# Optimization experiments

Hardware: AMD Instinct MI355X
Metric: run time of the kernel (lower is better)

## Reference

```python
import jax, jax.numpy as jnp
import numpy as np

N, E, D, K = 50000, 600000, 128, 8
EPS = 1e-09


def setup_inputs() -> dict:
    key = jax.random.key(0)
    ks = jax.random.split(key, 10)
    feature = jax.random.normal(ks[0], (N, D), dtype=jnp.float32)
    snorm_n = jax.random.uniform(ks[1], (N, 1), dtype=jnp.float32)
    src = jax.random.randint(ks[2], (E,), 0, N, dtype=jnp.int32)
    dst = jax.random.randint(ks[3], (E,), 0, N, dtype=jnp.int32)
    W_low = jax.random.normal(ks[4], (D, D), dtype=jnp.float32) / np.sqrt(D)
    W_high = jax.random.normal(ks[5], (D, D), dtype=jnp.float32) / np.sqrt(D)
    W_mid = jax.random.normal(ks[6], (D, D), dtype=jnp.float32) / np.sqrt(D)
    gamma_low = jax.random.uniform(ks[7], (K,), dtype=jnp.float32)
    gamma_high = jax.random.uniform(ks[8], (K,), dtype=jnp.float32)
    gamma_mid = jax.random.uniform(ks[9], (K,), dtype=jnp.float32)
    bias = jnp.zeros((D,), dtype=jnp.float32)
    return {"feature": feature, "snorm_n": snorm_n, "src": src, "dst": dst,
            "W_low": W_low, "W_high": W_high, "W_mid": W_mid,
            "gamma_low": gamma_low, "gamma_high": gamma_high,
            "gamma_mid": gamma_mid, "bias": bias}


def _mp(feat, src, dst, norm):
    # symmetric-normalized SpMM: h[v] = norm[v] * sum_{u->v} norm[u]*feat[u]
    msg = (feat * norm[:, None])[src]                        # [E, D] gather
    agg = jax.ops.segment_sum(msg, dst, num_segments=N)       # [N, D] scatter-add
    return agg * norm[:, None]


def reference(feature, snorm_n, src, dst, W_low, W_high, W_mid,
              gamma_low, gamma_high, gamma_mid, bias):
    deg = jax.ops.segment_sum(jnp.ones((E,), feature.dtype), dst, num_segments=N)
    norm = jnp.clip(deg, 1.0) ** -0.5                          # in-degree^-0.5
    alpha = jnp.linspace(EPS, 1.0 - EPS, K).astype(feature.dtype)
    midalpha = jnp.linspace(EPS, 1.0, K).astype(feature.dtype)

    h = _mp(feature, src, dst, norm)

    gl = jax.nn.relu(gamma_low)
    o0 = (jnp.dot(alpha, gl) * h + jnp.dot(1.0 - alpha, gl) * feature) @ W_low.T
    gh = jax.nn.relu(gamma_high)
    o1 = (jnp.dot(-alpha, gh) * h + jnp.dot(1.0 - alpha, gh) * feature) @ W_high.T
    gm = jax.nn.relu(gamma_mid)
    h1 = _mp(h, src, dst, norm)
    o2 = (jnp.sum(gm) * h1 - jnp.dot(midalpha, gm) * feature) @ W_mid.T

    # sequential mutual gating, exactly as the torch in-place updates
    o0 = o0 * jax.nn.sigmoid(o1 + o2)
    o1 = o1 * jax.nn.sigmoid(o0 + o2)
    o2 = o2 * jax.nn.sigmoid(o0 + o1)

    out = o0 + o1 + o2 + bias
    out = out * snorm_n          # graph_norm
    out = jax.nn.relu(out)       # activation
    return out
```

## Files before the change

kernel.cpp:

```cpp
#include <hip/hip_runtime.h>
#include <hip/hip_bf16.h>
#include <math.h>

#define N_NODES 50000
#define N_EDGES 600000
#define DIM 128
#define KGAM 8
#define EPSV 1e-9f

typedef __attribute__((ext_vector_type(8))) short short8;
typedef __attribute__((ext_vector_type(4))) float float4v;

__device__ __forceinline__ float bf2f(short s) {
    unsigned int u = ((unsigned int)(unsigned short)s) << 16;
    return __builtin_bit_cast(float, u);
}
__device__ __forceinline__ short f2bf(float f) {
    return (short)__builtin_bit_cast(unsigned short, __float2bfloat16(f));
}
__device__ __forceinline__ unsigned int pack2(float a, float b) {
    return (unsigned int)(unsigned short)f2bf(a) | ((unsigned int)(unsigned short)f2bf(b) << 16);
}
__device__ __forceinline__ float sigm(float x) { return 1.f / (1.f + __expf(-x)); }

__global__ void k_zero_int(int* __restrict__ p, int n) {
    int i = blockIdx.x * blockDim.x + threadIdx.x;
    if (i < n) p[i] = 0;
}

__global__ void k_deg(const int* __restrict__ dst, int* __restrict__ deg) {
    int e = blockIdx.x * blockDim.x + threadIdx.x;
    if (e < N_EDGES) atomicAdd(&deg[dst[e]], 1);
}

__global__ void k_scan1(const int* __restrict__ deg, int* __restrict__ rowstart,
                        int* __restrict__ bsums, float* __restrict__ norm) {
    __shared__ int s[256];
    int tid = threadIdx.x;
    int i0 = blockIdx.x * 1024 + tid * 4;
    int v[4]; int sum = 0;
#pragma unroll
    for (int c = 0; c < 4; ++c) {
        int i = i0 + c;
        int d = (i < N_NODES) ? deg[i] : 0;
        v[c] = d; sum += d;
    }
    s[tid] = sum; __syncthreads();
#pragma unroll
    for (int off = 1; off < 256; off <<= 1) {
        int t = (tid >= off) ? s[tid - off] : 0;
        __syncthreads();
        s[tid] += t;
        __syncthreads();
    }
    if (tid == 255) bsums[blockIdx.x] = s[255];
    int run = s[tid] - sum;
#pragma unroll
    for (int c = 0; c < 4; ++c) {
        int i = i0 + c;
        if (i < N_NODES) {
            rowstart[i] = run;
            norm[i] = rsqrtf((float)(v[c] < 1 ? 1 : v[c]));
        }
        run += v[c];
    }
}

__global__ void k_scan2(int* __restrict__ bsums, int nb) {
    __shared__ int s[64];
    int tid = threadIdx.x;
    int v = (tid < nb) ? bsums[tid] : 0;
    s[tid] = v; __syncthreads();
#pragma unroll
    for (int off = 1; off < 64; off <<= 1) {
        int t = (tid >= off) ? s[tid - off] : 0;
        __syncthreads();
        s[tid] += t;
        __syncthreads();
    }
    if (tid < nb) bsums[tid] = s[tid] - v;
}

__global__ void k_scan3(const int* __restrict__ bsums, int* __restrict__ rowstart) {
    int i = blockIdx.x * blockDim.x + threadIdx.x;
    if (i < N_NODES) rowstart[i] += bsums[i >> 10];
    if (i == 0) rowstart[N_NODES] = N_EDGES;
}

__global__ void k_fill(const int* __restrict__ src, const int* __restrict__ dst,
                       const int* __restrict__ rowstart, int* __restrict__ cnt,
                       int* __restrict__ esrc) {
    int e = blockIdx.x * blockDim.x + threadIdx.x;
    if (e < N_EDGES) {
        int d = dst[e];
        int slot = rowstart[d] + atomicAdd(&cnt[d], 1);
        esrc[slot] = src[e];
    }
}

__global__ void k_coeffs(const float* __restrict__ gl, const float* __restrict__ gh,
                         const float* __restrict__ gm, float* __restrict__ c) {
    if (threadIdx.x == 0 && blockIdx.x == 0) {
        float a0 = 0, b0 = 0, a1 = 0, b1 = 0, sg = 0, m2 = 0;
        for (int k = 0; k < KGAM; ++k) {
            float al = EPSV + (float)k * (1.f - 2.f * EPSV) / (KGAM - 1);
            float md = EPSV + (float)k * (1.f - EPSV) / (KGAM - 1);
            float l = fmaxf(gl[k], 0.f), h = fmaxf(gh[k], 0.f), m = fmaxf(gm[k], 0.f);
            a0 += al * l;  b0 += (1.f - al) * l;
            a1 += -al * h; b1 += (1.f - al) * h;
            sg += m;       m2 += md * m;
        }
        c[0] = a0; c[1] = b0; c[2] = a1; c[3] = b1; c[4] = sg; c[5] = -m2;
    }
}

__global__ void k_wconv(const float* __restrict__ W0, const float* __restrict__ W1,
                        const float* __restrict__ W2, const float* __restrict__ coeffs,
                        unsigned int* __restrict__ Wb) {
    int g = blockIdx.y;
    const float* Ws = (g < 2) ? W0 : (g < 4) ? W1 : W2;
    float c = coeffs[g];
    int i = (blockIdx.x * 256 + threadIdx.x) * 4;
    if (i < DIM * DIM) {
        float4 v = *(const float4*)(Ws + i);
        uint2 o; o.x = pack2(c * v.x, c * v.y); o.y = pack2(c * v.z, c * v.w);
        *(uint2*)(Wb + (g * DIM * DIM + i) / 2) = o;
    }
}

__global__ void k_prescale(const float4* __restrict__ f, const float* __restrict__ norm,
                           uint2* __restrict__ fb, uint2* __restrict__ fp) {
    int i = blockIdx.x * 256 + threadIdx.x;
    if (i >= N_NODES * DIM / 4) return;
    int row = i >> 5;
    float nv = norm[row];
    float4 v = f[i];
    uint2 a; a.x = pack2(v.x, v.y); a.y = pack2(v.z, v.w);
    uint2 b; b.x = pack2(v.x * nv, v.y * nv); b.y = pack2(v.z * nv, v.w * nv);
    fb[i] = a;
    fp[i] = b;
}

__device__ __forceinline__ void acc8(float* a, uint4 r) {
    a[0] += __builtin_bit_cast(float, r.x << 16);
    a[1] += __builtin_bit_cast(float, r.x & 0xffff0000u);
    a[2] += __builtin_bit_cast(float, r.y << 16);
    a[3] += __builtin_bit_cast(float, r.y & 0xffff0000u);
    a[4] += __builtin_bit_cast(float, r.z << 16);
    a[5] += __builtin_bit_cast(float, r.z & 0xffff0000u);
    a[6] += __builtin_bit_cast(float, r.w << 16);
    a[7] += __builtin_bit_cast(float, r.w & 0xffff0000u);
}

__global__ void k_spmm(const uint4* __restrict__ in, const float* __restrict__ norm,
                       const int* __restrict__ rowstart, const int* __restrict__ esrc,
                       uint4* __restrict__ hout, uint4* __restrict__ preout, int wpre) {
    int v = blockIdx.x * 16 + (threadIdx.x >> 4);
    int l = threadIdx.x & 15;
    if (v >= N_NODES) return;
    int beg = rowstart[v], end = rowstart[v + 1];
    float a[8] = {0.f, 0.f, 0.f, 0.f, 0.f, 0.f, 0.f, 0.f};
    int t = beg;
    for (; t + 3 < end; t += 4) {
        int u0 = esrc[t], u1 = esrc[t + 1], u2 = esrc[t + 2], u3 = esrc[t + 3];
        uint4 r0 = in[(size_t)u0 * 16 + l];
        uint4 r1 = in[(size_t)u1 * 16 + l];
        uint4 r2 = in[(size_t)u2 * 16 + l];
        uint4 r3 = in[(size_t)u3 * 16 + l];
        acc8(a, r0); acc8(a, r1); acc8(a, r2); acc8(a, r3);
    }
    for (; t < end; ++t) {
        uint4 r = in[(size_t)esrc[t] * 16 + l];
        acc8(a, r);
    }
    float nv = norm[v];
    uint4 o;
    o.x = pack2(a[0] * nv, a[1] * nv); o.y = pack2(a[2] * nv, a[3] * nv);
    o.z = pack2(a[4] * nv, a[5] * nv); o.w = pack2(a[6] * nv, a[7] * nv);
    hout[(size_t)v * 16 + l] = o;
    if (wpre) {
        float n2 = nv * nv;
        uint4 p;
        p.x = pack2(a[0] * n2, a[1] * n2); p.y = pack2(a[2] * n2, a[3] * n2);
        p.z = pack2(a[4] * n2, a[5] * n2); p.w = pack2(a[6] * n2, a[7] * n2);
        preout[(size_t)v * 16 + l] = p;
    }
}

#define RT 64

__global__ __launch_bounds__(512, 4) void k_gemm_fused(
    const short* __restrict__ hB, const short* __restrict__ fB,
    const short* __restrict__ h1B, const short* __restrict__ Wb,
    const float* __restrict__ bias, const float* __restrict__ snorm,
    float* __restrict__ out) {
    const int r0 = blockIdx.x * RT;
    const int tid = threadIdx.x;
    const int lane = tid & 63;
    const int ct = tid >> 6;
    const int m = lane & 15;
    const int quad = lane >> 4;

    float4v acc[3][4];
    const float4v zero = {0.f, 0.f, 0.f, 0.f};
#pragma unroll
    for (int g = 0; g < 3; ++g)
#pragma unroll
        for (int rt = 0; rt < 4; ++rt) acc[g][rt] = zero;

    const short* ah = hB  + (size_t)(r0 + m) * DIM + quad * 8;
    const short* af = fB  + (size_t)(r0 + m) * DIM + quad * 8;
    const short* a1 = h1B + (size_t)(r0 + m) * DIM + quad * 8;
    const short* wp = Wb  + (size_t)(ct * 16 + m) * DIM + quad * 8;

#pragma unroll
    for (int ks = 0; ks < 4; ++ks) {
        const int ko = ks * 32;
        short8 b0 = *(const short8*)(wp + ko);
        short8 b1 = *(const short8*)(wp + ko + DIM * DIM);
        short8 b2 = *(const short8*)(wp + ko + 2 * DIM * DIM);
        short8 b3 = *(const short8*)(wp + ko + 3 * DIM * DIM);
        short8 b4 = *(const short8*)(wp + ko + 4 * DIM * DIM);
        short8 b5 = *(const short8*)(wp + ko + 5 * DIM * DIM);
#pragma unroll
        for (int rt = 0; rt < 4; ++rt) {
            const int ro = rt * 16 * DIM + ko;
            short8 x_h = *(const short8*)(ah + ro);
            short8 x_f = *(const short8*)(af + ro);
            short8 x_1 = *(const short8*)(a1 + ro);
            acc[0][rt] = __builtin_amdgcn_mfma_f32_16x16x32_bf16(x_h, b0, acc[0][rt], 0, 0, 0);
            acc[0][rt] = __builtin_amdgcn_mfma_f32_16x16x32_bf16(x_f, b1, acc[0][rt], 0, 0, 0);
            acc[1][rt] = __builtin_amdgcn_mfma_f32_16x16x32_bf16(x_h, b2, acc[1][rt], 0, 0, 0);
            acc[1][rt] = __builtin_amdgcn_mfma_f32_16x16x32_bf16(x_f, b3, acc[1][rt], 0, 0, 0);
            acc[2][rt] = __builtin_amdgcn_mfma_f32_16x16x32_bf16(x_1, b4, acc[2][rt], 0, 0, 0);
            acc[2][rt] = __builtin_amdgcn_mfma_f32_16x16x32_bf16(x_f, b5, acc[2][rt], 0, 0, 0);
        }
    }

    const int col = ct * 16 + m;
    const float bc = bias[col];
#pragma unroll
    for (int rt = 0; rt < 4; ++rt) {
#pragma unroll
        for (int r = 0; r < 4; ++r) {
            int row = r0 + rt * 16 + quad * 4 + r;
            if (row < N_NODES) {
                float sn = snorm[row];
                float o0 = acc[0][rt][r], o1 = acc[1][rt][r], o2 = acc[2][rt][r];
                float g0 = o0 * sigm(o1 + o2);
                float g1 = o1 * sigm(g0 + o2);
                float g2 = o2 * sigm(g0 + g1);
                float vv = (g0 + g1 + g2 + bc) * sn;
                out[(size_t)row * DIM + col] = fmaxf(vv, 0.f);
            }
        }
    }
}

extern "C" void kernel_launch(void* const* d_in, const int* in_sizes, int n_in,
                              void* d_out, int out_size, void* d_ws, size_t ws_size,
                              hipStream_t stream) {
    const float* feature = (const float*)d_in[0];
    const float* snorm   = (const float*)d_in[1];
    const int*   src     = (const int*)d_in[2];
    const int*   dst     = (const int*)d_in[3];
    const float* W_low   = (const float*)d_in[4];
    const float* W_high  = (const float*)d_in[5];
    const float* W_mid   = (const float*)d_in[6];
    const float* gl      = (const float*)d_in[7];
    const float* gh      = (const float*)d_in[8];
    const float* gm      = (const float*)d_in[9];
    const float* bias    = (const float*)d_in[10];
    float* out = (float*)d_out;

    char* w = (char*)d_ws;
    auto alloc = [&](size_t bytes) {
        char* p = w;
        w += (bytes + 255) & ~(size_t)255;
        return p;
    };
    float* norm   = (float*)alloc((size_t)N_NODES * 4);
    int* deg      = (int*)alloc((size_t)2 * N_NODES * 4);
    int* cnt      = deg + N_NODES;
    int* rowstart = (int*)alloc((size_t)(N_NODES + 1) * 4);
    int* bsums    = (int*)alloc(64 * 4);
    int* esrc     = (int*)alloc((size_t)N_EDGES * 4);
    float* coeffs = (float*)alloc(64 * 4);
    short* Wb     = (short*)alloc((size_t)6 * DIM * DIM * 2);
    short* fb     = (short*)alloc((size_t)N_NODES * DIM * 2);
    short* fp     = (short*)alloc((size_t)N_NODES * DIM * 2);
    short* h      = (short*)alloc((size_t)N_NODES * DIM * 2);
    short* hp     = (short*)alloc((size_t)N_NODES * DIM * 2);
    short* h1     = (short*)alloc((size_t)N_NODES * DIM * 2);

    k_zero_int<<<(2 * N_NODES + 255) / 256, 256, 0, stream>>>(deg, 2 * N_NODES);
    k_deg<<<(N_EDGES + 255) / 256, 256, 0, stream>>>(dst, deg);
    int nchunks = (N_NODES + 1023) / 1024;
    k_scan1<<<nchunks, 256, 0, stream>>>(deg, rowstart, bsums, norm);
    k_scan2<<<1, 64, 0, stream>>>(bsums, nchunks);
    k_scan3<<<(N_NODES + 255) / 256, 256, 0, stream>>>(bsums, rowstart);
    k_fill<<<(N_EDGES + 255) / 256, 256, 0, stream>>>(src, dst, rowstart, cnt, esrc);
    k_coeffs<<<1, 1, 0, stream>>>(gl, gh, gm, coeffs);
    k_wconv<<<dim3(16, 6), 256, 0, stream>>>(W_low, W_high, W_mid, coeffs,
                                             (unsigned int*)Wb);
    k_prescale<<<(N_NODES * DIM / 4 + 255) / 256, 256, 0, stream>>>(
        (const float4*)feature, norm, (uint2*)fb, (uint2*)fp);

    int spmm_blocks = (N_NODES + 15) / 16;
    k_spmm<<<spmm_blocks, 256, 0, stream>>>((const uint4*)fp, norm, rowstart, esrc,
                                            (uint4*)h, (uint4*)hp, 1);
    k_spmm<<<spmm_blocks, 256, 0, stream>>>((const uint4*)hp, norm, rowstart, esrc,
                                            (uint4*)h1, (uint4*)hp, 0);

    k_gemm_fused<<<(N_NODES + RT - 1) / RT, 512, 0, stream>>>(
        h, fb, h1, Wb, bias, snorm, out);
}
```

Before: 288.7 us.

## Stage GEMM activations in LDS, unroll SpMM by 8, fold coeffs into wconv

The fused GEMM kernel now loads the block's h, feature and h1 tiles into shared memory once via global_load_lds. Previously all 8 waves re-read the same activation rows from global memory. The SpMM gather loop is unrolled to 8 outstanding row loads, with a 4/2/1 tail, to expose more memory parallelism. The single-thread coefficient kernel is folded into k_wconv and the zeroing kernel is replaced by hipMemsetAsync, removing two launches. The GEMM now uses 48KB of LDS per block, which may limit occupancy.

```diff
diff --git a/kernel.cpp b/kernel.cpp
--- a/kernel.cpp
+++ b/kernel.cpp
@@ -11,10 +11,6 @@
 typedef __attribute__((ext_vector_type(8))) short short8;
 typedef __attribute__((ext_vector_type(4))) float float4v;
 
-__device__ __forceinline__ float bf2f(short s) {
-    unsigned int u = ((unsigned int)(unsigned short)s) << 16;
-    return __builtin_bit_cast(float, u);
-}
 __device__ __forceinline__ short f2bf(float f) {
     return (short)__builtin_bit_cast(unsigned short, __float2bfloat16(f));
 }
@@ -22,11 +18,6 @@
     return (unsigned int)(unsigned short)f2bf(a) | ((unsigned int)(unsigned short)f2bf(b) << 16);
 }
 __device__ __forceinline__ float sigm(float x) { return 1.f / (1.f + __expf(-x)); }
-
-__global__ void k_zero_int(int* __restrict__ p, int n) {
-    int i = blockIdx.x * blockDim.x + threadIdx.x;
-    if (i < n) p[i] = 0;
-}
 
 __global__ void k_deg(const int* __restrict__ dst, int* __restrict__ deg) {
     int e = blockIdx.x * blockDim.x + threadIdx.x;
@@ -98,28 +89,24 @@
     }
 }
 
-__global__ void k_coeffs(const float* __restrict__ gl, const float* __restrict__ gh,
-                         const float* __restrict__ gm, float* __restrict__ c) {
-    if (threadIdx.x == 0 && blockIdx.x == 0) {
-        float a0 = 0, b0 = 0, a1 = 0, b1 = 0, sg = 0, m2 = 0;
-        for (int k = 0; k < KGAM; ++k) {
-            float al = EPSV + (float)k * (1.f - 2.f * EPSV) / (KGAM - 1);
-            float md = EPSV + (float)k * (1.f - EPSV) / (KGAM - 1);
-            float l = fmaxf(gl[k], 0.f), h = fmaxf(gh[k], 0.f), m = fmaxf(gm[k], 0.f);
-            a0 += al * l;  b0 += (1.f - al) * l;
-            a1 += -al * h; b1 += (1.f - al) * h;
-            sg += m;       m2 += md * m;
-        }
-        c[0] = a0; c[1] = b0; c[2] = a1; c[3] = b1; c[4] = sg; c[5] = -m2;
-    }
-}
-
 __global__ void k_wconv(const float* __restrict__ W0, const float* __restrict__ W1,
-                        const float* __restrict__ W2, const float* __restrict__ coeffs,
+                        const float* __restrict__ W2, const float* __restrict__ gl,
+                        const float* __restrict__ gh, const float* __restrict__ gm,
                         unsigned int* __restrict__ Wb) {
     int g = blockIdx.y;
+    float a0 = 0, b0 = 0, a1 = 0, b1 = 0, sg = 0, m2 = 0;
+#pragma unroll
+    for (int k = 0; k < KGAM; ++k) {
+        float al = EPSV + (float)k * (1.f - 2.f * EPSV) / (KGAM - 1);
+        float md = EPSV + (float)k * (1.f - EPSV) / (KGAM - 1);
+        float l = fmaxf(gl[k], 0.f), h = fmaxf(gh[k], 0.f), m = fmaxf(gm[k], 0.f);
+        a0 += al * l;  b0 += (1.f - al) * l;
+        a1 += -al * h; b1 += (1.f - al) * h;
+        sg += m;       m2 += md * m;
+    }
+    float cc[6] = {a0, b0, a1, b1, sg, -m2};
+    float c = cc[g];
     const float* Ws = (g < 2) ? W0 : (g < 4) ? W1 : W2;
-    float c = coeffs[g];
     int i = (blockIdx.x * 256 + threadIdx.x) * 4;
     if (i < DIM * DIM) {
         float4 v = *(const float4*)(Ws + i);
@@ -161,15 +148,37 @@
     int beg = rowstart[v], end = rowstart[v + 1];
     float a[8] = {0.f, 0.f, 0.f, 0.f, 0.f, 0.f, 0.f, 0.f};
     int t = beg;
-    for (; t + 3 < end; t += 4) {
+    for (; t + 7 < end; t += 8) {
+        int u0 = esrc[t],     u1 = esrc[t + 1], u2 = esrc[t + 2], u3 = esrc[t + 3];
+        int u4 = esrc[t + 4], u5 = esrc[t + 5], u6 = esrc[t + 6], u7 = esrc[t + 7];
+        uint4 r0 = in[(size_t)u0 * 16 + l];
+        uint4 r1 = in[(size_t)u1 * 16 + l];
+        uint4 r2 = in[(size_t)u2 * 16 + l];
+        uint4 r3 = in[(size_t)u3 * 16 + l];
+        uint4 r4 = in[(size_t)u4 * 16 + l];
+        uint4 r5 = in[(size_t)u5 * 16 + l];
+        uint4 r6 = in[(size_t)u6 * 16 + l];
+        uint4 r7 = in[(size_t)u7 * 16 + l];
+        acc8(a, r0); acc8(a, r1); acc8(a, r2); acc8(a, r3);
+        acc8(a, r4); acc8(a, r5); acc8(a, r6); acc8(a, r7);
+    }
+    if (t + 3 < end) {
         int u0 = esrc[t], u1 = esrc[t + 1], u2 = esrc[t + 2], u3 = esrc[t + 3];
         uint4 r0 = in[(size_t)u0 * 16 + l];
         uint4 r1 = in[(size_t)u1 * 16 + l];
         uint4 r2 = in[(size_t)u2 * 16 + l];
         uint4 r3 = in[(size_t)u3 * 16 + l];
         acc8(a, r0); acc8(a, r1); acc8(a, r2); acc8(a, r3);
-    }
-    for (; t < end; ++t) {
+        t += 4;
+    }
+    if (t + 1 < end) {
+        int u0 = esrc[t], u1 = esrc[t + 1];
+        uint4 r0 = in[(size_t)u0 * 16 + l];
+        uint4 r1 = in[(size_t)u1 * 16 + l];
+        acc8(a, r0); acc8(a, r1);
+        t += 2;
+    }
+    if (t < end) {
         uint4 r = in[(size_t)esrc[t] * 16 + l];
         acc8(a, r);
     }
@@ -189,18 +198,36 @@
 
 #define RT 64
 
+typedef const __attribute__((address_space(1))) unsigned int* gp1_t;
+typedef __attribute__((address_space(3))) unsigned int* lp3_t;
+
 __global__ __launch_bounds__(512, 4) void k_gemm_fused(
     const short* __restrict__ hB, const short* __restrict__ fB,
     const short* __restrict__ h1B, const short* __restrict__ Wb,
     const float* __restrict__ bias, const float* __restrict__ snorm,
     float* __restrict__ out) {
+    __shared__ short Ts[48 * 512];
+
     const int r0 = blockIdx.x * RT;
     const int tid = threadIdx.x;
     const int lane = tid & 63;
-    const int ct = tid >> 6;
+    const int wv = tid >> 6;
     const int m = lane & 15;
     const int quad = lane >> 4;
 
+#pragma unroll
+    for (int i = 0; i < 6; ++i) {
+        int s = wv * 6 + i;
+        int g = s >> 4, rt = (s >> 2) & 3, ks = s & 3;
+        const short* base = (g == 0) ? hB : (g == 1) ? fB : h1B;
+        int row = r0 + rt * 16 + m;
+        row = (row < N_NODES) ? row : (N_NODES - 1);
+        const short* gp = base + (size_t)row * DIM + ks * 32 + quad * 8;
+        __builtin_amdgcn_global_load_lds((gp1_t)(const void*)gp,
+                                         (lp3_t)(void*)&Ts[s * 512], 16, 0, 0);
+    }
+    __syncthreads();
+
     float4v acc[3][4];
     const float4v zero = {0.f, 0.f, 0.f, 0.f};
 #pragma unroll
@@ -208,11 +235,7 @@
 #pragma unroll
         for (int rt = 0; rt < 4; ++rt) acc[g][rt] = zero;
 
-    const short* ah = hB  + (size_t)(r0 + m) * DIM + quad * 8;
-    const short* af = fB  + (size_t)(r0 + m) * DIM + quad * 8;
-    const short* a1 = h1B + (size_t)(r0 + m) * DIM + quad * 8;
-    const short* wp = Wb  + (size_t)(ct * 16 + m) * DIM + quad * 8;
-
+    const short* wp = Wb + (size_t)(wv * 16 + m) * DIM + quad * 8;
 #pragma unroll
     for (int ks = 0; ks < 4; ++ks) {
         const int ko = ks * 32;
@@ -224,10 +247,10 @@
         short8 b5 = *(const short8*)(wp + ko + 5 * DIM * DIM);
 #pragma unroll
         for (int rt = 0; rt < 4; ++rt) {
-            const int ro = rt * 16 * DIM + ko;
-            short8 x_h = *(const short8*)(ah + ro);
-            short8 x_f = *(const short8*)(af + ro);
-            short8 x_1 = *(const short8*)(a1 + ro);
+            const short* ap = &Ts[(rt * 4 + ks) * 512 + lane * 8];
+            short8 x_h = *(const short8*)(ap);
+            short8 x_f = *(const short8*)(ap + 16 * 512);
+            short8 x_1 = *(const short8*)(ap + 32 * 512);
             acc[0][rt] = __builtin_amdgcn_mfma_f32_16x16x32_bf16(x_h, b0, acc[0][rt], 0, 0, 0);
             acc[0][rt] = __builtin_amdgcn_mfma_f32_16x16x32_bf16(x_f, b1, acc[0][rt], 0, 0, 0);
             acc[1][rt] = __builtin_amdgcn_mfma_f32_16x16x32_bf16(x_h, b2, acc[1][rt], 0, 0, 0);
@@ -237,7 +260,7 @@
         }
     }
 
-    const int col = ct * 16 + m;
+    const int col = wv * 16 + m;
     const float bc = bias[col];
 #pragma unroll
     for (int rt = 0; rt < 4; ++rt) {
@@ -285,7 +308,6 @@
     int* rowstart = (int*)alloc((size_t)(N_NODES + 1) * 4);
     int* bsums    = (int*)alloc(64 * 4);
     int* esrc     = (int*)alloc((size_t)N_EDGES * 4);
-    float* coeffs = (float*)alloc(64 * 4);
     short* Wb     = (short*)alloc((size_t)6 * DIM * DIM * 2);
     short* fb     = (short*)alloc((size_t)N_NODES * DIM * 2);
     short* fp     = (short*)alloc((size_t)N_NODES * DIM * 2);
@@ -293,15 +315,14 @@
     short* hp     = (short*)alloc((size_t)N_NODES * DIM * 2);
     short* h1     = (short*)alloc((size_t)N_NODES * DIM * 2);
 
-    k_zero_int<<<(2 * N_NODES + 255) / 256, 256, 0, stream>>>(deg, 2 * N_NODES);
+    hipMemsetAsync(deg, 0, (size_t)2 * N_NODES * 4, stream);
     k_deg<<<(N_EDGES + 255) / 256, 256, 0, stream>>>(dst, deg);
     int nchunks = (N_NODES + 1023) / 1024;
     k_scan1<<<nchunks, 256, 0, stream>>>(deg, rowstart, bsums, norm);
     k_scan2<<<1, 64, 0, stream>>>(bsums, nchunks);
     k_scan3<<<(N_NODES + 255) / 256, 256, 0, stream>>>(bsums, rowstart);
     k_fill<<<(N_EDGES + 255) / 256, 256, 0, stream>>>(src, dst, rowstart, cnt, esrc);
-    k_coeffs<<<1, 1, 0, stream>>>(gl, gh, gm, coeffs);
-    k_wconv<<<dim3(16, 6), 256, 0, stream>>>(W_low, W_high, W_mid, coeffs,
+    k_wconv<<<dim3(16, 6), 256, 0, stream>>>(W_low, W_high, W_mid, gl, gh, gm,
                                              (unsigned int*)Wb);
     k_prescale<<<(N_NODES * DIM / 4 + 255) / 256, 256, 0, stream>>>(
         (const float4*)feature, norm, (uint2*)fb, (uint2*)fp);
```

After: 256.5 us. 11.1% less time.
